# Kernel tuning notes

Hardware: AMD Instinct MI355X
Metric: run time of the kernel (lower is better)

Reference implementation:

```python
import jax, jax.numpy as jnp
import numpy as np

B, S, D = 4, 2048, 512
H = 8
HD = D // H  # 64
F = 2048
EPS = 1e-12


def _layer_norm(x, g, b):
    mu = jnp.mean(x, axis=-1, keepdims=True)
    var = jnp.mean((x - mu) ** 2, axis=-1, keepdims=True)
    return (x - mu) * jax.lax.rsqrt(var + EPS) * g + b


def setup_inputs() -> dict:
    key = jax.random.key(0)
    ks = jax.random.split(key, 16)
    sd = 0.02
    inp = {
        "x": jax.random.normal(ks[0], (B, S, D), dtype=jnp.float32),
        # per-head q/k/v projections stacked: [H, D, HD] weights, [H, HD] biases
        "Wq": jax.random.normal(ks[1], (H, D, HD), dtype=jnp.float32) * sd,
        "bq": jnp.zeros((H, HD), dtype=jnp.float32),
        "Wk": jax.random.normal(ks[2], (H, D, HD), dtype=jnp.float32) * sd,
        "bk": jnp.zeros((H, HD), dtype=jnp.float32),
        "Wv": jax.random.normal(ks[3], (H, D, HD), dtype=jnp.float32) * sd,
        "bv": jnp.zeros((H, HD), dtype=jnp.float32),
        "Wo": jax.random.normal(ks[4], (D, D), dtype=jnp.float32) * sd,
        "bo": jnp.zeros((D,), dtype=jnp.float32),
        "W1": jax.random.normal(ks[5], (D, F), dtype=jnp.float32) * sd,
        "b1": jnp.zeros((F,), dtype=jnp.float32),
        "W2": jax.random.normal(ks[6], (F, D), dtype=jnp.float32) * sd,
        "b2": jnp.zeros((D,), dtype=jnp.float32),
        "ln1_g": jnp.ones((D,), dtype=jnp.float32),
        "ln1_b": jnp.zeros((D,), dtype=jnp.float32),
        "ln2_g": jnp.ones((D,), dtype=jnp.float32),
        "ln2_b": jnp.zeros((D,), dtype=jnp.float32),
    }
    return inp


def reference(x, Wq, bq, Wk, bk, Wv, bv, Wo, bo, W1, b1, W2, b2,
              ln1_g, ln1_b, ln2_g, ln2_b):
    # Multi-head attention: per-head Linear projections, batched over heads.
    q = jnp.einsum('bsd,hde->bhse', x, Wq) + bq[None, :, None, :]
    k = jnp.einsum('bsd,hde->bhse', x, Wk) + bk[None, :, None, :]
    v = jnp.einsum('bsd,hde->bhse', x, Wv) + bv[None, :, None, :]
    scores = jnp.einsum('bhse,bhte->bhst', q, k) / jnp.sqrt(jnp.float32(HD))
    weights = jax.nn.softmax(scores, axis=-1)  # [B,H,S,S] -- dominant traffic
    attn = jnp.einsum('bhst,bhte->bhse', weights, v)
    # concat heads in order along feature dim -> [B,S,D]
    concat = jnp.transpose(attn, (0, 2, 1, 3)).reshape(B, S, D)
    attn_out = concat @ Wo + bo
    # post-LN residual 1
    x1 = _layer_norm(x + attn_out, ln1_g, ln1_b)
    # FFN (exact GELU, matching torch nn.GELU default)
    h = jax.nn.gelu(x1 @ W1 + b1, approximate=False)
    ff = h @ W2 + b2
    # post-LN residual 2
    return _layer_norm(x1 + ff, ln2_g, ln2_b)
```

## Files before the change

kernel.cpp:

```cpp
#include <hip/hip_runtime.h>
#include <math.h>

#define Bb 4
#define Ss 2048
#define Dd 512
#define Hh 8
#define HDd 64
#define Ff 2048

typedef __bf16 bf16x8 __attribute__((ext_vector_type(8)));
typedef float  f32x4  __attribute__((ext_vector_type(4)));

__device__ __forceinline__ float gelu_f(float x) {
    return 0.5f * x * (1.0f + erff(x * 0.70710678118654752440f));
}

__device__ __forceinline__ unsigned short bfbits(float f) {
    __bf16 h = (__bf16)f;
    return __builtin_bit_cast(unsigned short, h);
}

__device__ __forceinline__ void gld16(const unsigned short* g, unsigned short* l) {
    __builtin_amdgcn_global_load_lds(
        (const __attribute__((address_space(1))) unsigned int*)g,
        (__attribute__((address_space(3))) unsigned int*)l, 16, 0, 0);
}

__device__ __forceinline__ void tile_tconv(
    const float* __restrict__ in, unsigned short* __restrict__ out,
    int R, int C, int c0, int r0)
{
    __shared__ float tile[32][33];
    const int tx = threadIdx.x & 31, ty = threadIdx.x >> 5;
    #pragma unroll
    for (int rr = ty; rr < 32; rr += 8)
        tile[rr][tx] = in[(size_t)(r0 + rr) * C + c0 + tx];
    __syncthreads();
    #pragma unroll
    for (int cc = ty; cc < 32; cc += 8)
        out[(size_t)(c0 + cc) * R + r0 + tx] = bfbits(tile[tx][cc]);
}

__global__ __launch_bounds__(256) void prep_kernel(
    const float* __restrict__ Wq, const float* __restrict__ Wk,
    const float* __restrict__ Wv, const float* __restrict__ Wo,
    const float* __restrict__ W1, const float* __restrict__ W2,
    const float* __restrict__ x,
    unsigned short* __restrict__ WqT, unsigned short* __restrict__ WkT,
    unsigned short* __restrict__ WvT, unsigned short* __restrict__ WoT,
    unsigned short* __restrict__ W1T, unsigned short* __restrict__ W2T,
    unsigned short* __restrict__ xb)
{
    const int bid = blockIdx.x;
    if (bid < 768) {
        const float* src = bid < 256 ? Wq : (bid < 512 ? Wk : Wv);
        unsigned short* dst = bid < 256 ? WqT : (bid < 512 ? WkT : WvT);
        const int local = bid & 255;
        const int z = local >> 5;
        const int rem = local & 31;
        tile_tconv(src + (size_t)z * Dd * HDd, dst + (size_t)z * Dd * HDd,
                   Dd, HDd, (rem & 1) * 32, (rem >> 1) * 32);
    } else if (bid < 1024) {
        const int local = bid - 768;
        tile_tconv(Wo, WoT, Dd, Dd, (local & 15) * 32, (local >> 4) * 32);
    } else if (bid < 2048) {
        const int local = bid - 1024;
        tile_tconv(W1, W1T, Dd, Ff, (local & 63) * 32, (local >> 6) * 32);
    } else if (bid < 3072) {
        const int local = bid - 2048;
        tile_tconv(W2, W2T, Ff, Dd, (local & 15) * 32, (local >> 4) * 32);
    } else {
        const size_t i = ((size_t)(bid - 3072) * 256 + threadIdx.x) * 8;
        float4 a = *(const float4*)(x + i);
        float4 b = *(const float4*)(x + i + 4);
        union { unsigned short us[8]; uint4 u; } p;
        p.us[0] = bfbits(a.x); p.us[1] = bfbits(a.y);
        p.us[2] = bfbits(a.z); p.us[3] = bfbits(a.w);
        p.us[4] = bfbits(b.x); p.us[5] = bfbits(b.y);
        p.us[6] = bfbits(b.z); p.us[7] = bfbits(b.w);
        *(uint4*)(xb + i) = p.u;
    }
}

template<int ACT, int OUTBF>
__global__ __launch_bounds__(256) void gemm_mfma(
    const unsigned short* __restrict__ A, const unsigned short* __restrict__ Bt,
    const float* __restrict__ bias, void* __restrict__ C,
    int M, int N, int K)
{
    __shared__ unsigned short Asb[128 * 32];
    __shared__ unsigned short Bsb[128 * 32];
    const int t    = threadIdx.x;
    const int lane = t & 63;
    const int w    = t >> 6;
    const int ln15 = lane & 15;
    const int quad = lane >> 4;
    const int mw = (w & 1) * 64;
    const int nw = (w >> 1) * 64;
    const int m0 = blockIdx.y * 128;
    const int n0 = blockIdx.x * 128;

    const int r0c = t >> 2,           ch0 = (t & 3) << 3;
    const int r1c = (t + 256) >> 2,   ch1 = ch0;

    f32x4 acc[4][4];
    #pragma unroll
    for (int i = 0; i < 4; i++)
        #pragma unroll
        for (int j = 0; j < 4; j++) acc[i][j] = (f32x4){0.f, 0.f, 0.f, 0.f};

    for (int k0 = 0; k0 < K; k0 += 32) {
        gld16(A  + (size_t)(m0 + r0c) * K + k0 + ch0, &Asb[t * 8]);
        gld16(A  + (size_t)(m0 + r1c) * K + k0 + ch1, &Asb[(t + 256) * 8]);
        gld16(Bt + (size_t)(n0 + r0c) * K + k0 + ch0, &Bsb[t * 8]);
        gld16(Bt + (size_t)(n0 + r1c) * K + k0 + ch1, &Bsb[(t + 256) * 8]);
        __syncthreads();
        bf16x8 af[4], bf[4];
        const int kcol = quad * 8;
        #pragma unroll
        for (int i = 0; i < 4; i++)
            af[i] = *(const bf16x8*)&Asb[(mw + i * 16 + ln15) * 32 + kcol];
        #pragma unroll
        for (int j = 0; j < 4; j++)
            bf[j] = *(const bf16x8*)&Bsb[(nw + j * 16 + ln15) * 32 + kcol];
        #pragma unroll
        for (int i = 0; i < 4; i++)
            #pragma unroll
            for (int j = 0; j < 4; j++)
                acc[i][j] = __builtin_amdgcn_mfma_f32_16x16x32_bf16(
                    af[i], bf[j], acc[i][j], 0, 0, 0);
        __syncthreads();
    }

    #pragma unroll
    for (int i = 0; i < 4; i++) {
        #pragma unroll
        for (int r = 0; r < 4; r++) {
            const int m = m0 + mw + i * 16 + quad * 4 + r;
            #pragma unroll
            for (int j = 0; j < 4; j++) {
                const int n = n0 + nw + j * 16 + ln15;
                float val = acc[i][j][r] + bias[n];
                if (ACT) val = gelu_f(val);
                if (OUTBF)
                    ((unsigned short*)C)[(size_t)m * N + n] = bfbits(val);
                else
                    ((float*)C)[(size_t)m * N + n] = val;
            }
        }
    }
}

__global__ __launch_bounds__(256) void gemm_sk(
    const unsigned short* __restrict__ A, const unsigned short* __restrict__ Bt,
    const float* __restrict__ bias, float* __restrict__ C0, float* __restrict__ C1,
    int M, int N, int leadK, int Kslice)
{
    __shared__ unsigned short Asb[128 * 32];
    __shared__ unsigned short Bsb[128 * 32];
    const int t    = threadIdx.x;
    const int lane = t & 63;
    const int w    = t >> 6;
    const int ln15 = lane & 15;
    const int quad = lane >> 4;
    const int mw = (w & 1) * 64;
    const int nw = (w >> 1) * 64;
    const int m0 = blockIdx.y * 128;
    const int n0 = blockIdx.x * 128;
    const int z  = blockIdx.z;
    const int kbeg = z * Kslice;
    float* C = z ? C1 : C0;

    const int r0c = t >> 2,           ch0 = (t & 3) << 3;
    const int r1c = (t + 256) >> 2,   ch1 = ch0;

    f32x4 acc[4][4];
    #pragma unroll
    for (int i = 0; i < 4; i++)
        #pragma unroll
        for (int j = 0; j < 4; j++) acc[i][j] = (f32x4){0.f, 0.f, 0.f, 0.f};

    for (int k0 = kbeg; k0 < kbeg + Kslice; k0 += 32) {
        gld16(A  + (size_t)(m0 + r0c) * leadK + k0 + ch0, &Asb[t * 8]);
        gld16(A  + (size_t)(m0 + r1c) * leadK + k0 + ch1, &Asb[(t + 256) * 8]);
        gld16(Bt + (size_t)(n0 + r0c) * leadK + k0 + ch0, &Bsb[t * 8]);
        gld16(Bt + (size_t)(n0 + r1c) * leadK + k0 + ch1, &Bsb[(t + 256) * 8]);
        __syncthreads();
        bf16x8 af[4], bf[4];
        const int kcol = quad * 8;
        #pragma unroll
        for (int i = 0; i < 4; i++)
            af[i] = *(const bf16x8*)&Asb[(mw + i * 16 + ln15) * 32 + kcol];
        #pragma unroll
        for (int j = 0; j < 4; j++)
            bf[j] = *(const bf16x8*)&Bsb[(nw + j * 16 + ln15) * 32 + kcol];
        #pragma unroll
        for (int i = 0; i < 4; i++)
            #pragma unroll
            for (int j = 0; j < 4; j++)
                acc[i][j] = __builtin_amdgcn_mfma_f32_16x16x32_bf16(
                    af[i], bf[j], acc[i][j], 0, 0, 0);
        __syncthreads();
    }

    #pragma unroll
    for (int i = 0; i < 4; i++) {
        #pragma unroll
        for (int r = 0; r < 4; r++) {
            const int m = m0 + mw + i * 16 + quad * 4 + r;
            #pragma unroll
            for (int j = 0; j < 4; j++) {
                const int n = n0 + nw + j * 16 + ln15;
                const float val = acc[i][j][r] + (z == 0 ? bias[n] : 0.f);
                C[(size_t)m * N + n] = val;
            }
        }
    }
}

__global__ __launch_bounds__(256) void qkv_mfma(
    const unsigned short* __restrict__ A,
    const unsigned short* __restrict__ WqT, const unsigned short* __restrict__ WkT,
    const unsigned short* __restrict__ WvT,
    const float* __restrict__ bq, const float* __restrict__ bk,
    const float* __restrict__ bv, unsigned short* __restrict__ qkv)
{
    const unsigned short* Bt = blockIdx.z == 0 ? WqT : (blockIdx.z == 1 ? WkT : WvT);
    const float* bias = blockIdx.z == 0 ? bq : (blockIdx.z == 1 ? bk : bv);
    unsigned short* O = qkv + (size_t)blockIdx.z * ((size_t)Bb * Hh * Ss * HDd);
    const float scl = blockIdx.z == 0 ? 0.125f * 1.44269504088896341f : 1.0f;

    __shared__ unsigned short Asb[128 * 32];
    __shared__ unsigned short Bsb[128 * 32];
    const int t    = threadIdx.x;
    const int lane = t & 63;
    const int w    = t >> 6;
    const int ln15 = lane & 15;
    const int quad = lane >> 4;
    const int mw = (w & 1) * 64;
    const int nw = (w >> 1) * 64;
    const int m0 = blockIdx.y * 128;
    const int n0 = blockIdx.x * 128;

    const int r0c = t >> 2,         ch0 = (t & 3) << 3;
    const int r1c = (t + 256) >> 2, ch1 = ch0;

    f32x4 acc[4][4];
    #pragma unroll
    for (int i = 0; i < 4; i++)
        #pragma unroll
        for (int j = 0; j < 4; j++) acc[i][j] = (f32x4){0.f, 0.f, 0.f, 0.f};

    for (int k0 = 0; k0 < Dd; k0 += 32) {
        gld16(A  + (size_t)(m0 + r0c) * Dd + k0 + ch0, &Asb[t * 8]);
        gld16(A  + (size_t)(m0 + r1c) * Dd + k0 + ch1, &Asb[(t + 256) * 8]);
        gld16(Bt + (size_t)(n0 + r0c) * Dd + k0 + ch0, &Bsb[t * 8]);
        gld16(Bt + (size_t)(n0 + r1c) * Dd + k0 + ch1, &Bsb[(t + 256) * 8]);
        __syncthreads();
        bf16x8 af[4], bf[4];
        const int kcol = quad * 8;
        #pragma unroll
        for (int i = 0; i < 4; i++)
            af[i] = *(const bf16x8*)&Asb[(mw + i * 16 + ln15) * 32 + kcol];
        #pragma unroll
        for (int j = 0; j < 4; j++)
            bf[j] = *(const bf16x8*)&Bsb[(nw + j * 16 + ln15) * 32 + kcol];
        #pragma unroll
        for (int i = 0; i < 4; i++)
            #pragma unroll
            for (int j = 0; j < 4; j++)
                acc[i][j] = __builtin_amdgcn_mfma_f32_16x16x32_bf16(
                    af[i], bf[j], acc[i][j], 0, 0, 0);
        __syncthreads();
    }

    if (blockIdx.z == 2) {
        #pragma unroll
        for (int i = 0; i < 4; i++) {
            const int mb = m0 + mw + i * 16 + quad * 4;
            const int bI = mb >> 11;
            const int sI = mb & 2047;
            #pragma unroll
            for (int j = 0; j < 4; j++) {
                const int n = n0 + nw + j * 16 + ln15;
                union { unsigned short us[4]; uint2 u2; } pk;
                #pragma unroll
                for (int r = 0; r < 4; r++)
                    pk.us[r] = bfbits(acc[i][j][r] + bias[n]);
                *(uint2*)&O[(((size_t)bI * Hh + (n >> 6)) * HDd + (n & 63)) * Ss + sI]
                    = pk.u2;
            }
        }
    } else {
        #pragma unroll
        for (int i = 0; i < 4; i++) {
            #pragma unroll
            for (int r = 0; r < 4; r++) {
                const int m  = m0 + mw + i * 16 + quad * 4 + r;
                const int bI = m >> 11;
                const int sI = m & 2047;
                #pragma unroll
                for (int j = 0; j < 4; j++) {
                    const int n = n0 + nw + j * 16 + ln15;
                    const float val = (acc[i][j][r] + bias[n]) * scl;
                    O[(((size_t)bI * Hh + (n >> 6)) * Ss + sI) * HDd + (n & 63)] =
                        bfbits(val);
                }
            }
        }
    }
}

__global__ __launch_bounds__(256) void attn_mfma(
    const unsigned short* __restrict__ q, const unsigned short* __restrict__ k,
    const unsigned short* __restrict__ vt, unsigned short* __restrict__ out)
{
    __shared__ unsigned short Ks[64][72];
    __shared__ unsigned short VTs[64][72];
    __shared__ unsigned short Ps[64][72];
    __shared__ float lrow[4][16];
    const int t    = threadIdx.x;
    const int lane = t & 63;
    const int w    = t >> 6;
    const int ln15 = lane & 15;
    const int quad = lane >> 4;
    const int qw   = w * 16;
    const int h = blockIdx.y, b = blockIdx.z;
    const int q0 = blockIdx.x * 64;
    const unsigned short* qb  = q  + (((size_t)b * Hh + h) * Ss + q0) * HDd;
    const unsigned short* kb  = k  + ((size_t)b * Hh + h) * Ss * HDd;
    const unsigned short* vtb = vt + ((size_t)b * Hh + h) * HDd * Ss;

    const bf16x8 qf0 = *(const bf16x8*)(qb + (size_t)(qw + ln15) * HDd + quad * 8);
    const bf16x8 qf1 = *(const bf16x8*)(qb + (size_t)(qw + ln15) * HDd + 32 + quad * 8);

    f32x4 o_acc[4];
    #pragma unroll
    for (int s = 0; s < 4; s++) o_acc[s] = (f32x4){0.f, 0.f, 0.f, 0.f};
    float l_run = 0.f;

    for (int kt = 0; kt < Ss; kt += 64) {
        __syncthreads();
        #pragma unroll
        for (int p = 0; p < 2; p++) {
            const int u = p * 256 + t;
            const int row = u >> 3, ch = u & 7;
            *(bf16x8*)&Ks[row][ch * 8] =
                *(const bf16x8*)(kb + (size_t)(kt + row) * HDd + ch * 8);
            *(bf16x8*)&VTs[row][ch * 8] =
                *(const bf16x8*)(vtb + (size_t)row * Ss + kt + ch * 8);
        }
        __syncthreads();

        f32x4 sc[4];
        #pragma unroll
        for (int s = 0; s < 4; s++) {
            const bf16x8 ka  = *(const bf16x8*)&Ks[s * 16 + ln15][quad * 8];
            const bf16x8 kb2 = *(const bf16x8*)&Ks[s * 16 + ln15][32 + quad * 8];
            f32x4 z = (f32x4){0.f, 0.f, 0.f, 0.f};
            z = __builtin_amdgcn_mfma_f32_16x16x32_bf16(ka, qf0, z, 0, 0, 0);
            sc[s] = __builtin_amdgcn_mfma_f32_16x16x32_bf16(kb2, qf1, z, 0, 0, 0);
        }

        #pragma unroll
        for (int s = 0; s < 4; s++)
            #pragma unroll
            for (int r = 0; r < 4; r++) {
                sc[s][r] = exp2f(sc[s][r]);
                l_run += sc[s][r];
            }

        #pragma unroll
        for (int s = 0; s < 4; s++) {
            union { unsigned short us[4]; uint2 u2; } pk;
            #pragma unroll
            for (int r = 0; r < 4; r++) pk.us[r] = bfbits(sc[s][r]);
            *(uint2*)&Ps[qw + ln15][s * 16 + quad * 4] = pk.u2;
        }

        const bf16x8 pf0 = *(const bf16x8*)&Ps[qw + ln15][quad * 8];
        const bf16x8 pf1 = *(const bf16x8*)&Ps[qw + ln15][32 + quad * 8];
        #pragma unroll
        for (int s = 0; s < 4; s++) {
            const bf16x8 v0 = *(const bf16x8*)&VTs[s * 16 + ln15][quad * 8];
            const bf16x8 v1 = *(const bf16x8*)&VTs[s * 16 + ln15][32 + quad * 8];
            o_acc[s] = __builtin_amdgcn_mfma_f32_16x16x32_bf16(pf0, v0, o_acc[s], 0, 0, 0);
            o_acc[s] = __builtin_amdgcn_mfma_f32_16x16x32_bf16(pf1, v1, o_acc[s], 0, 0, 0);
        }
    }

    l_run += __shfl_xor(l_run, 16);
    l_run += __shfl_xor(l_run, 32);
    if (quad == 0) lrow[w][ln15] = l_run;
    const float4 lv = *(const float4*)&lrow[w][quad * 4];
    const float inv[4] = {1.f / lv.x, 1.f / lv.y, 1.f / lv.z, 1.f / lv.w};
    #pragma unroll
    for (int r = 0; r < 4; r++) {
        const int row = q0 + qw + quad * 4 + r;
        #pragma unroll
        for (int s = 0; s < 4; s++) {
            const int dim = s * 16 + ln15;
            out[((size_t)b * Ss + row) * Dd + h * HDd + dim] =
                bfbits(o_acc[s][r] * inv[r]);
        }
    }
}

template<int WRITE_BF>
__global__ __launch_bounds__(256) void ln_kernel(
    const float* __restrict__ a0, const float* __restrict__ a1,
    const float* __restrict__ res,
    const float* __restrict__ g, const float* __restrict__ bb,
    float* __restrict__ out, unsigned short* __restrict__ outb)
{
    const int row = blockIdx.x;
    const int t = threadIdx.x;
    const size_t o0 = (size_t)row * Dd + t;
    const size_t o1 = o0 + 256;
    float v0 = a0[o0] + a1[o0] + res[o0];
    float v1 = a0[o1] + a1[o1] + res[o1];

    float sum = v0 + v1;
    #pragma unroll
    for (int o = 32; o; o >>= 1) sum += __shfl_down(sum, o);
    __shared__ float red1[4], red2[4];
    const int wid = t >> 6, lane = t & 63;
    if (!lane) red1[wid] = sum;
    __syncthreads();
    sum = red1[0] + red1[1] + red1[2] + red1[3];
    const float mu = sum * (1.0f / Dd);

    const float d0 = v0 - mu, d1 = v1 - mu;
    float sq = d0 * d0 + d1 * d1;
    #pragma unroll
    for (int o = 32; o; o >>= 1) sq += __shfl_down(sq, o);
    if (!lane) red2[wid] = sq;
    __syncthreads();
    sq = red2[0] + red2[1] + red2[2] + red2[3];
    const float rstd = rsqrtf(sq * (1.0f / Dd) + 1e-12f);

    const float y0 = d0 * rstd * g[t] + bb[t];
    const float y1 = d1 * rstd * g[t + 256] + bb[t + 256];
    out[o0] = y0;
    out[o1] = y1;
    if (WRITE_BF) {
        outb[o0] = bfbits(y0);
        outb[o1] = bfbits(y1);
    }
}

extern "C" void kernel_launch(void* const* d_in, const int* in_sizes, int n_in,
                              void* d_out, int out_size, void* d_ws, size_t ws_size,
                              hipStream_t stream) {
    const float* x   = (const float*)d_in[0];
    const float* Wq  = (const float*)d_in[1];
    const float* bq  = (const float*)d_in[2];
    const float* Wk  = (const float*)d_in[3];
    const float* bk  = (const float*)d_in[4];
    const float* Wv  = (const float*)d_in[5];
    const float* bv  = (const float*)d_in[6];
    const float* Wo  = (const float*)d_in[7];
    const float* bo  = (const float*)d_in[8];
    const float* W1  = (const float*)d_in[9];
    const float* b1  = (const float*)d_in[10];
    const float* W2  = (const float*)d_in[11];
    const float* b2  = (const float*)d_in[12];
    const float* g1  = (const float*)d_in[13];
    const float* be1 = (const float*)d_in[14];
    const float* g2  = (const float*)d_in[15];
    const float* be2 = (const float*)d_in[16];
    float* out = (float*)d_out;

    const size_t NT = (size_t)Bb * Ss * Dd;
    unsigned short* wsu = (unsigned short*)d_ws;
    unsigned short* qkvb = wsu;
    float* projA = (float*)(wsu + 3 * NT);
    float* projB = projA + NT;
    unsigned short* hb   = wsu + 3 * NT;
    unsigned short* actb = wsu + 7 * NT;
    unsigned short* x1b  = wsu + 8 * NT;
    float* ff0 = (float*)(wsu + 7 * NT);
    float* ff1 = (float*)wsu;
    float* x1  = (float*)(wsu + 9 * NT);
    unsigned short* wpool = wsu + 11 * NT;
    unsigned short* WqT = wpool;
    unsigned short* WkT = wpool + 262144;
    unsigned short* WvT = wpool + 524288;
    unsigned short* WoT = wpool + 786432;
    unsigned short* W1T = wpool + 1048576;
    unsigned short* W2T = wpool + 2097152;
    const int M = Bb * Ss;

    prep_kernel<<<5120, 256, 0, stream>>>(
        Wq, Wk, Wv, Wo, W1, W2, x,
        WqT, WkT, WvT, WoT, W1T, W2T, actb);

    qkv_mfma<<<dim3(Dd / 128, M / 128, 3), 256, 0, stream>>>(
        actb, WqT, WkT, WvT, bq, bk, bv, qkvb);

    attn_mfma<<<dim3(Ss / 64, Hh, Bb), 256, 0, stream>>>(
        qkvb, qkvb + NT, qkvb + 2 * NT, actb);

    gemm_sk<<<dim3(Dd / 128, M / 128, 2), 256, 0, stream>>>(
        actb, WoT, bo, projA, projB, M, Dd, Dd, Dd / 2);

    ln_kernel<1><<<M, 256, 0, stream>>>(projA, projB, x, g1, be1, x1, x1b);

    gemm_mfma<1, 1><<<dim3(Ff / 128, M / 128), 256, 0, stream>>>(
        x1b, W1T, b1, hb, M, Ff, Dd);

    gemm_sk<<<dim3(Dd / 128, M / 128, 2), 256, 0, stream>>>(
        hb, W2T, b2, ff0, ff1, M, Dd, Ff, Ff / 2);

    ln_kernel<0><<<M, 256, 0, stream>>>(ff0, ff1, x1, g2, be2, out, nullptr);
}
```

Baseline: 334.2 us.

## Store split-K GEMM partials in bf16 and stage attention K/V via LDS DMA

The split-K projection GEMMs now write their two partial sums as bf16 instead of fp32, and the layer-norm kernel reads and widens them. This halves the write and read traffic of the intermediate partials, at some cost in precision because each partial is rounded before the residual add. Separately, the attention kernel loads K and V^T tiles into unpadded shared arrays with global_load_lds instead of register-staged vector copies. Dropping the padding may add LDS bank conflicts on the fragment reads.

```diff
diff --git a/kernel.cpp b/kernel.cpp
--- a/kernel.cpp
+++ b/kernel.cpp
@@ -18,6 +18,10 @@
 __device__ __forceinline__ unsigned short bfbits(float f) {
     __bf16 h = (__bf16)f;
     return __builtin_bit_cast(unsigned short, h);
+}
+
+__device__ __forceinline__ float b2f(unsigned short u) {
+    return (float)__builtin_bit_cast(__bf16, u);
 }
 
 __device__ __forceinline__ void gld16(const unsigned short* g, unsigned short* l) {
@@ -153,7 +157,8 @@
 
 __global__ __launch_bounds__(256) void gemm_sk(
     const unsigned short* __restrict__ A, const unsigned short* __restrict__ Bt,
-    const float* __restrict__ bias, float* __restrict__ C0, float* __restrict__ C1,
+    const float* __restrict__ bias,
+    unsigned short* __restrict__ C0, unsigned short* __restrict__ C1,
     int M, int N, int leadK, int Kslice)
 {
     __shared__ unsigned short Asb[128 * 32];
@@ -169,7 +174,7 @@
     const int n0 = blockIdx.x * 128;
     const int z  = blockIdx.z;
     const int kbeg = z * Kslice;
-    float* C = z ? C1 : C0;
+    unsigned short* C = z ? C1 : C0;
 
     const int r0c = t >> 2,           ch0 = (t & 3) << 3;
     const int r1c = (t + 256) >> 2,   ch1 = ch0;
@@ -212,7 +217,7 @@
             for (int j = 0; j < 4; j++) {
                 const int n = n0 + nw + j * 16 + ln15;
                 const float val = acc[i][j][r] + (z == 0 ? bias[n] : 0.f);
-                C[(size_t)m * N + n] = val;
+                C[(size_t)m * N + n] = bfbits(val);
             }
         }
     }
@@ -315,8 +320,8 @@
     const unsigned short* __restrict__ q, const unsigned short* __restrict__ k,
     const unsigned short* __restrict__ vt, unsigned short* __restrict__ out)
 {
-    __shared__ unsigned short Ks[64][72];
-    __shared__ unsigned short VTs[64][72];
+    __shared__ unsigned short Ks[64 * 64];
+    __shared__ unsigned short VTs[64 * 64];
     __shared__ unsigned short Ps[64][72];
     __shared__ float lrow[4][16];
     const int t    = threadIdx.x;
@@ -331,6 +336,9 @@
     const unsigned short* kb  = k  + ((size_t)b * Hh + h) * Ss * HDd;
     const unsigned short* vtb = vt + ((size_t)b * Hh + h) * HDd * Ss;
 
+    const int sr0 = t >> 3,         sch0 = (t & 7) << 3;
+    const int sr1 = (t + 256) >> 3, sch1 = sch0;
+
     const bf16x8 qf0 = *(const bf16x8*)(qb + (size_t)(qw + ln15) * HDd + quad * 8);
     const bf16x8 qf1 = *(const bf16x8*)(qb + (size_t)(qw + ln15) * HDd + 32 + quad * 8);
 
@@ -341,22 +349,17 @@
 
     for (int kt = 0; kt < Ss; kt += 64) {
         __syncthreads();
-        #pragma unroll
-        for (int p = 0; p < 2; p++) {
-            const int u = p * 256 + t;
-            const int row = u >> 3, ch = u & 7;
-            *(bf16x8*)&Ks[row][ch * 8] =
-                *(const bf16x8*)(kb + (size_t)(kt + row) * HDd + ch * 8);
-            *(bf16x8*)&VTs[row][ch * 8] =
-                *(const bf16x8*)(vtb + (size_t)row * Ss + kt + ch * 8);
-        }
+        gld16(kb  + (size_t)(kt + sr0) * HDd + sch0, &Ks[t * 8]);
+        gld16(kb  + (size_t)(kt + sr1) * HDd + sch1, &Ks[(t + 256) * 8]);
+        gld16(vtb + (size_t)sr0 * Ss + kt + sch0, &VTs[t * 8]);
+        gld16(vtb + (size_t)sr1 * Ss + kt + sch1, &VTs[(t + 256) * 8]);
         __syncthreads();
 
         f32x4 sc[4];
         #pragma unroll
         for (int s = 0; s < 4; s++) {
-            const bf16x8 ka  = *(const bf16x8*)&Ks[s * 16 + ln15][quad * 8];
-            const bf16x8 kb2 = *(const bf16x8*)&Ks[s * 16 + ln15][32 + quad * 8];
+            const bf16x8 ka  = *(const bf16x8*)&Ks[(s * 16 + ln15) * 64 + quad * 8];
+            const bf16x8 kb2 = *(const bf16x8*)&Ks[(s * 16 + ln15) * 64 + 32 + quad * 8];
             f32x4 z = (f32x4){0.f, 0.f, 0.f, 0.f};
             z = __builtin_amdgcn_mfma_f32_16x16x32_bf16(ka, qf0, z, 0, 0, 0);
             sc[s] = __builtin_amdgcn_mfma_f32_16x16x32_bf16(kb2, qf1, z, 0, 0, 0);
@@ -382,8 +385,8 @@
         const bf16x8 pf1 = *(const bf16x8*)&Ps[qw + ln15][32 + quad * 8];
         #pragma unroll
         for (int s = 0; s < 4; s++) {
-            const bf16x8 v0 = *(const bf16x8*)&VTs[s * 16 + ln15][quad * 8];
-            const bf16x8 v1 = *(const bf16x8*)&VTs[s * 16 + ln15][32 + quad * 8];
+            const bf16x8 v0 = *(const bf16x8*)&VTs[(s * 16 + ln15) * 64 + quad * 8];
+            const bf16x8 v1 = *(const bf16x8*)&VTs[(s * 16 + ln15) * 64 + 32 + quad * 8];
             o_acc[s] = __builtin_amdgcn_mfma_f32_16x16x32_bf16(pf0, v0, o_acc[s], 0, 0, 0);
             o_acc[s] = __builtin_amdgcn_mfma_f32_16x16x32_bf16(pf1, v1, o_acc[s], 0, 0, 0);
         }
@@ -408,7 +411,7 @@
 
 template<int WRITE_BF>
 __global__ __launch_bounds__(256) void ln_kernel(
-    const float* __restrict__ a0, const float* __restrict__ a1,
+    const unsigned short* __restrict__ a0, const unsigned short* __restrict__ a1,
     const float* __restrict__ res,
     const float* __restrict__ g, const float* __restrict__ bb,
     float* __restrict__ out, unsigned short* __restrict__ outb)
@@ -417,8 +420,8 @@
     const int t = threadIdx.x;
     const size_t o0 = (size_t)row * Dd + t;
     const size_t o1 = o0 + 256;
-    float v0 = a0[o0] + a1[o0] + res[o0];
-    float v1 = a0[o1] + a1[o1] + res[o1];
+    float v0 = b2f(a0[o0]) + b2f(a1[o0]) + res[o0];
+    float v1 = b2f(a0[o1]) + b2f(a1[o1]) + res[o1];
 
     float sum = v0 + v1;
     #pragma unroll
@@ -473,15 +476,15 @@
 
     const size_t NT = (size_t)Bb * Ss * Dd;
     unsigned short* wsu = (unsigned short*)d_ws;
-    unsigned short* qkvb = wsu;
-    float* projA = (float*)(wsu + 3 * NT);
-    float* projB = projA + NT;
-    unsigned short* hb   = wsu + 3 * NT;
-    unsigned short* actb = wsu + 7 * NT;
-    unsigned short* x1b  = wsu + 8 * NT;
-    float* ff0 = (float*)(wsu + 7 * NT);
-    float* ff1 = (float*)wsu;
-    float* x1  = (float*)(wsu + 9 * NT);
+    unsigned short* qkvb  = wsu;
+    unsigned short* projA = wsu + 3 * NT;
+    unsigned short* projB = wsu + 4 * NT;
+    unsigned short* hb    = wsu + 3 * NT;
+    unsigned short* actb  = wsu + 7 * NT;
+    unsigned short* x1b   = wsu + 8 * NT;
+    unsigned short* ff0   = wsu;
+    unsigned short* ff1   = wsu + NT;
+    float* x1 = (float*)(wsu + 9 * NT);
     unsigned short* wpool = wsu + 11 * NT;
     unsigned short* WqT = wpool;
     unsigned short* WkT = wpool + 262144;
```

New measurement: 336.2 us. Within noise of the previous version (+0.6%).
